# Optimization experiments

Hardware: AMD Instinct MI355X
Metric: run time of the kernel (lower is better)

Reference implementation:

```python
import jax, jax.numpy as jnp
import numpy as np

NS, NV = 48, 10                    # scalar / vector multiplicities (cfg.ns, cfg.nv)
WN = NS * NS + NS * NV             # per-edge TP weight numel: paths 0e*0e->0e and 0e*1o->1o
OUT = NS + 3 * NV                  # out irreps 48x0e + 10x1o -> 78 dims
INV = float(1.0 / np.sqrt(NS))     # e3nn-style path normalization (fan_in = mul_in)
N_LIG, N_REC, N_ATOM = 2000, 2000, 15000
E_LL, E_RR, E_AA = 15000, 10000, 15000
E_LR, E_LA, E_AR = 5000, 8000, 8000


def setup_inputs() -> dict:
    key = jax.random.key(0)
    ks = jax.random.split(key, 40)
    f = lambda i, shape, s=1.0: jax.random.normal(ks[i], shape, dtype=jnp.float32) * s
    ii = lambda i, n, e: jax.random.randint(ks[i], (e,), 0, n, dtype=jnp.int32)
    w_s = (1.0 / (3 * NS)) ** 0.5
    return {
        'lig_x': f(0, (N_LIG, NS)), 'rec_x': f(1, (N_REC, NS)), 'atom_x': f(2, (N_ATOM, NS)),
        'll_attr': f(3, (E_LL, NS)), 'rr_attr': f(4, (E_RR, NS)), 'aa_attr': f(5, (E_AA, NS)),
        'lr_attr': f(6, (E_LR, NS)), 'la_attr': f(7, (E_LA, NS)), 'ar_attr': f(8, (E_AR, NS)),
        'll_sh': f(9, (E_LL, 9)), 'rr_sh': f(10, (E_RR, 9)), 'aa_sh': f(11, (E_AA, 9)),
        'lr_sh': f(12, (E_LR, 9)), 'la_sh': f(13, (E_LA, 9)), 'ar_sh': f(14, (E_AR, 9)),
        'mlp_w1': f(15, (9, 3 * NS, 3 * NS), w_s), 'mlp_b1': jnp.zeros((9, 3 * NS), jnp.float32),
        'mlp_w2': f(16, (9, 3 * NS, 3 * NS), w_s), 'mlp_b2': jnp.zeros((9, 3 * NS), jnp.float32),
        'mlp_w3': f(17, (9, 3 * NS, WN), w_s), 'mlp_b3': jnp.zeros((9, WN), jnp.float32),
        'll_src': ii(18, N_LIG, E_LL), 'll_dst': ii(19, N_LIG, E_LL),
        'rr_src': ii(20, N_REC, E_RR), 'rr_dst': ii(21, N_REC, E_RR),
        'aa_src': ii(22, N_ATOM, E_AA), 'aa_dst': ii(23, N_ATOM, E_AA),
        'lr_lig': ii(24, N_LIG, E_LR), 'lr_rec': ii(25, N_REC, E_LR),
        'la_lig': ii(26, N_LIG, E_LA), 'la_atom': ii(27, N_ATOM, E_LA),
        'ar_atom': ii(28, N_ATOM, E_AR), 'ar_rec': ii(29, N_REC, E_AR),
    }


def _tp_conv(src_x, dst_x, e_attr, e_sh, src_idx, dst_idx, n_dst, w1, b1, w2, b2, w3, b3):
    """FullyConnectedTensorProductConv: per-edge MLP -> TP weights, CG tensor
    product of gathered source features with edge SH, mean scatter to dst."""
    fs = src_x[src_idx]                                          # (E, ns) gather
    z = jnp.concatenate([e_attr, fs, dst_x[dst_idx]], axis=-1)
    h = jax.nn.relu(z @ w1 + b1)
    h = jax.nn.relu(h @ w2 + b2)
    w = h @ w3 + b3                                              # (E, WN) edge-conditioned TP weights
    w0 = w[:, : NS * NS].reshape(-1, NS, NS)                     # 0e x 0e -> 0e path
    wv = w[:, NS * NS :].reshape(-1, NS, NV)                     # 0e x 1o -> 1o path
    out0 = jnp.einsum('ei,eio->eo', fs, w0) * e_sh[:, :1] * INV  # (E, ns)
    outv = jnp.einsum('ei,eiv,em->evm', fs, wv, e_sh[:, 1:4]) * INV  # (E, nv, 3)
    msg = jnp.concatenate([out0, outv.reshape(-1, NV * 3)], axis=-1)
    agg = jax.ops.segment_sum(msg, dst_idx, num_segments=n_dst)
    deg = jax.ops.segment_sum(jnp.ones((msg.shape[0], 1), msg.dtype), dst_idx, num_segments=n_dst)
    return agg / jnp.maximum(deg, 1.0)                           # mean reduction


def reference(lig_x, rec_x, atom_x, ll_attr, rr_attr, aa_attr, lr_attr, la_attr, ar_attr,
              ll_sh, rr_sh, aa_sh, lr_sh, la_sh, ar_sh,
              mlp_w1, mlp_b1, mlp_w2, mlp_b2, mlp_w3, mlp_b3,
              ll_src, ll_dst, rr_src, rr_dst, aa_src, aa_dst,
              lr_lig, lr_rec, la_lig, la_atom, ar_atom, ar_rec):
    P = lambda c: (mlp_w1[c], mlp_b1[c], mlp_w2[c], mlp_b2[c], mlp_w3[c], mlp_b3[c])
    # one interaction layer = 9 structurally distinct convs (lig/rec/atom intra + 6 cross dirs)
    lig_u = (_tp_conv(lig_x, lig_x, ll_attr, ll_sh, ll_src, ll_dst, N_LIG, *P(0))
           + _tp_conv(rec_x, lig_x, lr_attr, lr_sh, lr_rec, lr_lig, N_LIG, *P(1))
           + _tp_conv(atom_x, lig_x, la_attr, la_sh, la_atom, la_lig, N_LIG, *P(2)))
    rec_u = (_tp_conv(lig_x, rec_x, lr_attr, lr_sh, lr_lig, lr_rec, N_REC, *P(3))
           + _tp_conv(rec_x, rec_x, rr_attr, rr_sh, rr_src, rr_dst, N_REC, *P(4))
           + _tp_conv(atom_x, rec_x, ar_attr, ar_sh, ar_atom, ar_rec, N_REC, *P(5)))
    atom_u = (_tp_conv(lig_x, atom_x, la_attr, la_sh, la_lig, la_atom, N_ATOM, *P(6))
            + _tp_conv(rec_x, atom_x, ar_attr, ar_sh, ar_rec, ar_atom, N_ATOM, *P(7))
            + _tp_conv(atom_x, atom_x, aa_attr, aa_sh, aa_src, aa_dst, N_ATOM, *P(8)))
    pad = lambda x: jnp.pad(x, ((0, 0), (0, OUT - NS)))          # residual: pad scalars to out irreps
    return jnp.concatenate([pad(lig_x) + lig_u, pad(rec_x) + rec_u, pad(atom_x) + atom_u], axis=0)
```

## Files before the change

kernel.cpp:

```cpp
#include <hip/hip_runtime.h>


namespace {

constexpr int NCONV = 9;
constexpr int ETOT  = 82000;
constexpr float INV = 0.14433756729740643f;

constexpr int EC[NCONV]     = {15000,5000,8000,5000,10000,8000,8000,8000,15000};
constexpr int NBLKC[NCONV]  = {118,40,63,40,79,63,63,63,118};
constexpr int EOFF[NCONV]   = {0,15000,20000,28000,33000,43000,51000,59000,67000};
constexpr int DEGOFF[NCONV] = {0,2000,4000,6000,8000,10000,12000,27000,42000};
constexpr int NBLK_TOT = 647;

typedef _Float16 f16;
typedef __attribute__((ext_vector_type(8))) _Float16 f16x8;
typedef __attribute__((ext_vector_type(4))) float f32x4;

#define MFMA(a, b, c) __builtin_amdgcn_mfma_f32_16x16x32_f16((a), (b), (c), 0, 0, 0)

struct ConvPtrs {
  const float* src_x[NCONV];
  const float* dst_x[NCONV];
  const float* attr[NCONV];
  const float* sh[NCONV];
  const int*   sidx[NCONV];
  const int*   didx[NCONV];
};

}

__device__ __forceinline__ int conv_decode(int bid, int& rem) {
  int c = 0; rem = bid;
  while (c < NCONV - 1 && rem >= NBLKC[c]) { rem -= NBLKC[c]; ++c; }
  return c;
}

__global__ __launch_bounds__(64) void prep_w12(
    const float* __restrict__ w1, const float* __restrict__ b1,
    const float* __restrict__ w2, const float* __restrict__ b2,
    f16* __restrict__ w1f, f16* __restrict__ w2f) {
  const int b = blockIdx.x;
  const int sel = b >= 405, bb = sel ? b - 405 : b;
  const int c = bb / 45, r2 = bb % 45, cb = r2 / 5, s = r2 % 5;
  const float* w  = sel ? w2 : w1;
  const float* bi = sel ? b2 : b1;
  f16* dst = (sel ? w2f : w1f) + ((size_t)(c * 9 + cb) * 5 + s) * 512;
  const int l = threadIdx.x;
  const int n = cb * 16 + (l & 15);
  f16x8 pack;
#pragma unroll
  for (int j = 0; j < 8; ++j) {
    const int k = s * 32 + ((l >> 4) << 3) + j;
    float v = 0.f;
    if (k < 144)       v = w[((size_t)c * 144 + k) * 144 + n];
    else if (k == 144) v = bi[c * 144 + n];
    pack[j] = (f16)v;
  }
  ((f16x8*)dst)[l] = pack;
}

__global__ __launch_bounds__(256) void prep_w3k(
    const float* __restrict__ w3, const float* __restrict__ b3,
    f16* __restrict__ w3f) {
  const int b = blockIdx.x;
  const int c = b / 48, i = b % 48;
  const float* wc = w3 + (size_t)c * 144 * 2784;
  const float* bc = b3 + (size_t)c * 2784;
  f16* dst = w3f + (size_t)(c * 48 + i) * 20 * 512;
#pragma unroll 1
  for (int it = 0; it < 40; ++it) {
    const int f = it * 256 + threadIdx.x;
    const int s = f >> 11, g2 = f & 2047, cb = g2 >> 9, l = (g2 >> 3) & 63, j = f & 7;
    const int k = s * 32 + ((l >> 4) << 3) + j;
    const int col = cb * 16 + (l & 15);
    float v = 0.f;
    if (k <= 144) {
      const float* src = (k == 144) ? bc : (wc + (size_t)k * 2784);
      if (col < 48)      v = src[i * 48 + col];
      else if (col < 58) v = src[2304 + i * 10 + (col - 48)];
    }
    dst[f] = (f16)v;
  }
}

__global__ __launch_bounds__(256) void deg_kernel(ConvPtrs P, float* __restrict__ deg) {
  const int gid = blockIdx.x * 256 + threadIdx.x;
  if (gid >= ETOT) return;
  int c = 0;
  while (c < NCONV - 1 && gid >= EOFF[c + 1]) ++c;
  const int e = gid - EOFF[c];
  atomicAdd(&deg[DEGOFF[c] + P.didx[c][e]], 1.0f);
}

__global__ __launch_bounds__(256) void resid_kernel(
    const float* __restrict__ lig, const float* __restrict__ rec,
    const float* __restrict__ atom, float* __restrict__ out) {
  const int gid = blockIdx.x * 256 + threadIdx.x;
  if (gid >= 19000 * 78) return;
  const int row = gid / 78, j = gid - row * 78;
  const float* x; int node;
  if (row < 2000)      { x = lig;  node = row; }
  else if (row < 4000) { x = rec;  node = row - 2000; }
  else                 { x = atom; node = row - 4000; }
  out[gid] = (j < 48) ? x[(size_t)node * 48 + j] : 0.f;
}

template<int NCB, int CB0>
__device__ __forceinline__ void layer_mm(
    const f16x8* __restrict__ Av, const f16x8* __restrict__ wv,
    int c, int lane, int wr, f32x4 acc[4][5]) {
  f16x8 B[NCB][5];
#pragma unroll
  for (int cb = 0; cb < NCB; ++cb)
#pragma unroll
    for (int s = 0; s < 5; ++s)
      B[cb][s] = wv[((size_t)(c * 9 + CB0 + cb) * 5 + s) * 64 + lane];
#pragma unroll
  for (int rb = 0; rb < 4; ++rb)
#pragma unroll
    for (int cb = 0; cb < NCB; ++cb) acc[rb][cb] = (f32x4)0.0f;
#pragma unroll
  for (int s = 0; s < 5; ++s) {
    f16x8 A[4];
#pragma unroll
    for (int rb = 0; rb < 4; ++rb) A[rb] = Av[((wr * 4 + rb) * 5 + s) * 64 + lane];
#pragma unroll
    for (int rb = 0; rb < 4; ++rb)
#pragma unroll
      for (int cb = 0; cb < NCB; ++cb)
        acc[rb][cb] = MFMA(A[rb], B[cb][s], acc[rb][cb]);
  }
}

template<int NCB, int CB0>
__device__ __forceinline__ void layer_wb(const f32x4 acc[4][5], f16* __restrict__ At,
                                         int lane, int wr) {
#pragma unroll
  for (int cb = 0; cb < NCB; ++cb) {
    const int k = (CB0 + cb) * 16 + (lane & 15);
    const int s = k >> 5, g = (k >> 3) & 3, j = k & 7;
#pragma unroll
    for (int rb = 0; rb < 4; ++rb)
#pragma unroll
      for (int r = 0; r < 4; ++r) {
        const int row = ((lane >> 4) << 2) + r;
        At[((((wr * 4 + rb) * 5 + s) * 4 + g) * 16 + row) * 8 + j] =
            (f16)fmaxf(acc[rb][cb][r], 0.f);
      }
  }
}

#define BILIN_STEP(i, CUR, NXT)                                                   \
  {                                                                               \
    if ((i) + 1 < 48) {                                                           \
      const size_t fb = (size_t)(c * 48 + (i) + 1) * 20;                          \
      _Pragma("unroll") for (int s = 0; s < 5; ++s)                               \
        _Pragma("unroll") for (int cb = 0; cb < 2; ++cb)                          \
          Bb##NXT[cb][s] = w3v[(fb + s * 4 + (wc * 2 + cb)) * 64 + lane];         \
    }                                                                             \
    f32x4 T[4][2];                                                                \
    _Pragma("unroll") for (int rb = 0; rb < 4; ++rb)                              \
      _Pragma("unroll") for (int cb = 0; cb < 2; ++cb) T[rb][cb] = (f32x4)0.0f;   \
    _Pragma("unroll") for (int s = 0; s < 5; ++s)                                 \
      _Pragma("unroll") for (int rb = 0; rb < 4; ++rb)                            \
        _Pragma("unroll") for (int cb = 0; cb < 2; ++cb)                          \
          T[rb][cb] = MFMA(Af[rb][s], Bb##CUR[cb][s], T[rb][cb]);                 \
    _Pragma("unroll") for (int rb = 0; rb < 4; ++rb) {                            \
      const f32x4 fs4 =                                                           \
          *(const f32x4*)&fst[i][wr * 64 + rb * 16 + ((lane >> 4) << 2)];         \
      _Pragma("unroll") for (int cb = 0; cb < 2; ++cb)                            \
        msg[rb][cb] += fs4 * T[rb][cb];                                           \
    }                                                                             \
  }

__global__ __launch_bounds__(256, 2) void fused_conv(
    ConvPtrs P, const f16* __restrict__ w1f, const f16* __restrict__ w2f,
    const f16* __restrict__ w3f, const float* __restrict__ deg,
    float* __restrict__ out) {
  __shared__ f16   Atile[20480];
  __shared__ float fst[48][128];
  __shared__ float shb[128][4];
  __shared__ int   sidb[128], dstb[128];
  __shared__ float invdegb[128];

  int rem; const int c = conv_decode(blockIdx.x, rem);
  const int E = EC[c], e0 = rem * 128;
  const int tid = threadIdx.x, lane = tid & 63, w = tid >> 6;
  const int wr = w >> 1, wc = w & 1;

  if (tid < 128) {
    int ec = e0 + tid; if (ec >= E) ec = E - 1;
    sidb[tid] = P.sidx[c][ec];
    const int d = P.didx[c][ec]; dstb[tid] = d;
    const float* shp = P.sh[c] + (size_t)ec * 9;
    shb[tid][0] = shp[0]; shb[tid][1] = shp[1];
    shb[tid][2] = shp[2]; shb[tid][3] = shp[3];
    invdegb[tid] = 1.f / fmaxf(deg[DEGOFF[c] + d], 1.f);
  }
  __syncthreads();

  {
    const float* attr = P.attr[c];
    const float* sx = P.src_x[c];
    const float* dx = P.dst_x[c];
#pragma unroll 1
    for (int it = 0; it < 10; ++it) {
      const int u = it * 256 + tid, j8 = u >> 7, e = u & 127;
      int ec = e0 + e; if (ec >= E) ec = E - 1;
      float v[8];
      if (j8 < 6) {
        const float* p = attr + (size_t)ec * 48 + j8 * 8;
#pragma unroll
        for (int t = 0; t < 8; ++t) v[t] = p[t];
      } else if (j8 < 12) {
        const float* p = sx + (size_t)sidb[e] * 48 + (j8 - 6) * 8;
#pragma unroll
        for (int t = 0; t < 8; ++t) v[t] = p[t];
#pragma unroll
        for (int t = 0; t < 8; ++t) fst[(j8 - 6) * 8 + t][e] = v[t];
      } else if (j8 < 18) {
        const float* p = dx + (size_t)dstb[e] * 48 + (j8 - 12) * 8;
#pragma unroll
        for (int t = 0; t < 8; ++t) v[t] = p[t];
      } else if (j8 == 18) {
        v[0] = 1.f;
#pragma unroll
        for (int t = 1; t < 8; ++t) v[t] = 0.f;
      } else {
#pragma unroll
        for (int t = 0; t < 8; ++t) v[t] = 0.f;
      }
      f16x8 h;
#pragma unroll
      for (int t = 0; t < 8; ++t) h[t] = (f16)v[t];
      const int s = j8 >> 2, g = j8 & 3, rbg = e >> 4, row = e & 15;
      ((f16x8*)Atile)[((rbg * 5 + s) * 4 + g) * 16 + row] = h;
    }
  }
  __syncthreads();

  const f16x8* Av  = (const f16x8*)Atile;
  const f16x8* w1v = (const f16x8*)w1f;
  const f16x8* w2v = (const f16x8*)w2f;
  const f16x8* w3v = (const f16x8*)w3f;

  f32x4 acc[4][5];
  if (wc == 0) layer_mm<5, 0>(Av, w1v, c, lane, wr, acc);
  else         layer_mm<4, 5>(Av, w1v, c, lane, wr, acc);
  __syncthreads();
  if (wc == 0) layer_wb<5, 0>(acc, Atile, lane, wr);
  else         layer_wb<4, 5>(acc, Atile, lane, wr);
  __syncthreads();
  if (wc == 0) layer_mm<5, 0>(Av, w2v, c, lane, wr, acc);
  else         layer_mm<4, 5>(Av, w2v, c, lane, wr, acc);
  __syncthreads();
  if (wc == 0) layer_wb<5, 0>(acc, Atile, lane, wr);
  else         layer_wb<4, 5>(acc, Atile, lane, wr);
  __syncthreads();

  f16x8 Af[4][5];
#pragma unroll
  for (int rb = 0; rb < 4; ++rb)
#pragma unroll
    for (int s = 0; s < 5; ++s)
      Af[rb][s] = Av[((wr * 4 + rb) * 5 + s) * 64 + lane];

  f32x4 msg[4][2];
#pragma unroll
  for (int rb = 0; rb < 4; ++rb)
#pragma unroll
    for (int cb = 0; cb < 2; ++cb) msg[rb][cb] = (f32x4)0.0f;

  f16x8 Bb0[2][5], Bb1[2][5];
  {
    const size_t fb = (size_t)(c * 48) * 20;
#pragma unroll
    for (int s = 0; s < 5; ++s)
#pragma unroll
      for (int cb = 0; cb < 2; ++cb)
        Bb0[cb][s] = w3v[(fb + s * 4 + (wc * 2 + cb)) * 64 + lane];
  }
#pragma unroll 1
  for (int ii = 0; ii < 48; ii += 2) {
    BILIN_STEP(ii, 0, 1);
    BILIN_STEP(ii + 1, 1, 0);
  }

  const int outbase = (c < 3) ? 0 : (c < 6 ? 2000 : 4000);
#pragma unroll
  for (int rb = 0; rb < 4; ++rb)
#pragma unroll
    for (int r = 0; r < 4; ++r) {
      const int el = wr * 64 + rb * 16 + ((lane >> 4) << 2) + r;
      if (e0 + el >= E) continue;
      const float sc = invdegb[el] * INV;
      float* op = out + ((size_t)outbase + dstb[el]) * 78;
      const float s0 = shb[el][0], s1 = shb[el][1], s2 = shb[el][2], s3 = shb[el][3];
#pragma unroll
      for (int cb = 0; cb < 2; ++cb) {
        const int col = (wc * 2 + cb) * 16 + (lane & 15);
        const float v = msg[rb][cb][r] * sc;
        if (col < 48) {
          atomicAdd(op + col, v * s0);
        } else if (col < 58) {
          const int vv = col - 48;
          atomicAdd(op + 48 + vv * 3 + 0, v * s1);
          atomicAdd(op + 48 + vv * 3 + 1, v * s2);
          atomicAdd(op + 48 + vv * 3 + 2, v * s3);
        }
      }
    }
}

extern "C" void kernel_launch(void* const* d_in, const int* in_sizes, int n_in,
                              void* d_out, int out_size, void* d_ws, size_t ws_size,
                              hipStream_t stream) {
  (void)in_sizes; (void)n_in; (void)out_size; (void)ws_size;
  const float* lig_x  = (const float*)d_in[0];
  const float* rec_x  = (const float*)d_in[1];
  const float* atom_x = (const float*)d_in[2];
  const float* attr_ll = (const float*)d_in[3];
  const float* attr_rr = (const float*)d_in[4];
  const float* attr_aa = (const float*)d_in[5];
  const float* attr_lr = (const float*)d_in[6];
  const float* attr_la = (const float*)d_in[7];
  const float* attr_ar = (const float*)d_in[8];
  const float* sh_ll = (const float*)d_in[9];
  const float* sh_rr = (const float*)d_in[10];
  const float* sh_aa = (const float*)d_in[11];
  const float* sh_lr = (const float*)d_in[12];
  const float* sh_la = (const float*)d_in[13];
  const float* sh_ar = (const float*)d_in[14];
  const float* w1 = (const float*)d_in[15];
  const float* b1 = (const float*)d_in[16];
  const float* w2 = (const float*)d_in[17];
  const float* b2 = (const float*)d_in[18];
  const float* w3 = (const float*)d_in[19];
  const float* b3 = (const float*)d_in[20];
  const int* ll_src = (const int*)d_in[21];
  const int* ll_dst = (const int*)d_in[22];
  const int* rr_src = (const int*)d_in[23];
  const int* rr_dst = (const int*)d_in[24];
  const int* aa_src = (const int*)d_in[25];
  const int* aa_dst = (const int*)d_in[26];
  const int* lr_lig = (const int*)d_in[27];
  const int* lr_rec = (const int*)d_in[28];
  const int* la_lig = (const int*)d_in[29];
  const int* la_atom = (const int*)d_in[30];
  const int* ar_atom = (const int*)d_in[31];
  const int* ar_rec  = (const int*)d_in[32];

  f16* w1f = (f16*)d_ws;
  f16* w2f = w1f + 207360;
  f16* w3f = w2f + 207360;
  float* deg = (float*)(w3f + 4423680);

  ConvPtrs P;
  const float* SX[NCONV] = {lig_x, rec_x, atom_x, lig_x, rec_x, atom_x, lig_x, rec_x, atom_x};
  const float* DX[NCONV] = {lig_x, lig_x, lig_x, rec_x, rec_x, rec_x, atom_x, atom_x, atom_x};
  const float* AT[NCONV] = {attr_ll, attr_lr, attr_la, attr_lr, attr_rr, attr_ar, attr_la, attr_ar, attr_aa};
  const float* SH[NCONV] = {sh_ll, sh_lr, sh_la, sh_lr, sh_rr, sh_ar, sh_la, sh_ar, sh_aa};
  const int*   SI[NCONV] = {ll_src, lr_rec, la_atom, lr_lig, rr_src, ar_atom, la_lig, ar_rec, aa_src};
  const int*   DI[NCONV] = {ll_dst, lr_lig, la_lig, lr_rec, rr_dst, ar_rec, la_atom, ar_atom, aa_dst};
  for (int cc = 0; cc < NCONV; ++cc) {
    P.src_x[cc] = SX[cc]; P.dst_x[cc] = DX[cc]; P.attr[cc] = AT[cc];
    P.sh[cc] = SH[cc]; P.sidx[cc] = SI[cc]; P.didx[cc] = DI[cc];
  }

  prep_w12<<<810, 64, 0, stream>>>(w1, b1, w2, b2, w1f, w2f);
  prep_w3k<<<432, 256, 0, stream>>>(w3, b3, w3f);
  hipMemsetAsync(deg, 0, 57000 * sizeof(float), stream);
  deg_kernel<<<(ETOT + 255) / 256, 256, 0, stream>>>(P, deg);
  resid_kernel<<<(19000 * 78 + 255) / 256, 256, 0, stream>>>(lig_x, rec_x, atom_x, (float*)d_out);
  fused_conv<<<NBLK_TOT, 256, 0, stream>>>(P, w1f, w2f, w3f, deg, (float*)d_out);
}
```

Before: 212.2 us.

## Stream W3 tiles through LDS with async loads and raise occupancy to three blocks

```diff
diff --git a/kernel.cpp b/kernel.cpp
--- a/kernel.cpp
+++ b/kernel.cpp
@@ -15,6 +15,7 @@
 
 typedef _Float16 f16;
 typedef __attribute__((ext_vector_type(8))) _Float16 f16x8;
+typedef __attribute__((ext_vector_type(4))) _Float16 f16x4;
 typedef __attribute__((ext_vector_type(4))) float f32x4;
 
 #define MFMA(a, b, c) __builtin_amdgcn_mfma_f32_16x16x32_f16((a), (b), (c), 0, 0, 0)
@@ -34,6 +35,16 @@
   int c = 0; rem = bid;
   while (c < NCONV - 1 && rem >= NBLKC[c]) { rem -= NBLKC[c]; ++c; }
   return c;
+}
+
+__device__ __forceinline__ void gld_lds16(const void* g, void* l) {
+  __builtin_amdgcn_global_load_lds(
+      (const __attribute__((address_space(1))) void*)g,
+      (__attribute__((address_space(3))) void*)l, 16, 0, 0);
+}
+
+__device__ __forceinline__ f32x4 cvt4(f16x4 h) {
+  return (f32x4){(float)h[0], (float)h[1], (float)h[2], (float)h[3]};
 }
 
 __global__ __launch_bounds__(64) void prep_w12(
@@ -110,18 +121,16 @@
 __device__ __forceinline__ void layer_mm(
     const f16x8* __restrict__ Av, const f16x8* __restrict__ wv,
     int c, int lane, int wr, f32x4 acc[4][5]) {
-  f16x8 B[NCB][5];
-#pragma unroll
-  for (int cb = 0; cb < NCB; ++cb)
-#pragma unroll
-    for (int s = 0; s < 5; ++s)
-      B[cb][s] = wv[((size_t)(c * 9 + CB0 + cb) * 5 + s) * 64 + lane];
 #pragma unroll
   for (int rb = 0; rb < 4; ++rb)
 #pragma unroll
     for (int cb = 0; cb < NCB; ++cb) acc[rb][cb] = (f32x4)0.0f;
 #pragma unroll
   for (int s = 0; s < 5; ++s) {
+    f16x8 B[NCB];
+#pragma unroll
+    for (int cb = 0; cb < NCB; ++cb)
+      B[cb] = wv[((size_t)(c * 9 + CB0 + cb) * 5 + s) * 64 + lane];
     f16x8 A[4];
 #pragma unroll
     for (int rb = 0; rb < 4; ++rb) A[rb] = Av[((wr * 4 + rb) * 5 + s) * 64 + lane];
@@ -129,7 +138,7 @@
     for (int rb = 0; rb < 4; ++rb)
 #pragma unroll
       for (int cb = 0; cb < NCB; ++cb)
-        acc[rb][cb] = MFMA(A[rb], B[cb][s], acc[rb][cb]);
+        acc[rb][cb] = MFMA(A[rb], B[cb], acc[rb][cb]);
   }
 }
 
@@ -151,38 +160,15 @@
   }
 }
 
-#define BILIN_STEP(i, CUR, NXT)                                                   \
-  {                                                                               \
-    if ((i) + 1 < 48) {                                                           \
-      const size_t fb = (size_t)(c * 48 + (i) + 1) * 20;                          \
-      _Pragma("unroll") for (int s = 0; s < 5; ++s)                               \
-        _Pragma("unroll") for (int cb = 0; cb < 2; ++cb)                          \
-          Bb##NXT[cb][s] = w3v[(fb + s * 4 + (wc * 2 + cb)) * 64 + lane];         \
-    }                                                                             \
-    f32x4 T[4][2];                                                                \
-    _Pragma("unroll") for (int rb = 0; rb < 4; ++rb)                              \
-      _Pragma("unroll") for (int cb = 0; cb < 2; ++cb) T[rb][cb] = (f32x4)0.0f;   \
-    _Pragma("unroll") for (int s = 0; s < 5; ++s)                                 \
-      _Pragma("unroll") for (int rb = 0; rb < 4; ++rb)                            \
-        _Pragma("unroll") for (int cb = 0; cb < 2; ++cb)                          \
-          T[rb][cb] = MFMA(Af[rb][s], Bb##CUR[cb][s], T[rb][cb]);                 \
-    _Pragma("unroll") for (int rb = 0; rb < 4; ++rb) {                            \
-      const f32x4 fs4 =                                                           \
-          *(const f32x4*)&fst[i][wr * 64 + rb * 16 + ((lane >> 4) << 2)];         \
-      _Pragma("unroll") for (int cb = 0; cb < 2; ++cb)                            \
-        msg[rb][cb] += fs4 * T[rb][cb];                                           \
-    }                                                                             \
-  }
-
-__global__ __launch_bounds__(256, 2) void fused_conv(
+__global__ __launch_bounds__(256, 3) void fused_conv(
     ConvPtrs P, const f16* __restrict__ w1f, const f16* __restrict__ w2f,
     const f16* __restrict__ w3f, const float* __restrict__ deg,
     float* __restrict__ out) {
-  __shared__ f16   Atile[20480];
-  __shared__ float fst[48][128];
-  __shared__ float shb[128][4];
-  __shared__ int   sidb[128], dstb[128];
-  __shared__ float invdegb[128];
+  __shared__ __align__(16) char smem[54272];
+  f16* Atile = (f16*)smem;
+  f16 (*fst)[128] = (f16 (*)[128])(smem + 40960);
+  int* sidb = (int*)(smem + 53248);
+  int* dstb = (int*)(smem + 53760);
 
   int rem; const int c = conv_decode(blockIdx.x, rem);
   const int E = EC[c], e0 = rem * 128;
@@ -192,11 +178,7 @@
   if (tid < 128) {
     int ec = e0 + tid; if (ec >= E) ec = E - 1;
     sidb[tid] = P.sidx[c][ec];
-    const int d = P.didx[c][ec]; dstb[tid] = d;
-    const float* shp = P.sh[c] + (size_t)ec * 9;
-    shb[tid][0] = shp[0]; shb[tid][1] = shp[1];
-    shb[tid][2] = shp[2]; shb[tid][3] = shp[3];
-    invdegb[tid] = 1.f / fmaxf(deg[DEGOFF[c] + d], 1.f);
+    dstb[tid] = P.didx[c][ec];
   }
   __syncthreads();
 
@@ -218,7 +200,7 @@
 #pragma unroll
         for (int t = 0; t < 8; ++t) v[t] = p[t];
 #pragma unroll
-        for (int t = 0; t < 8; ++t) fst[(j8 - 6) * 8 + t][e] = v[t];
+        for (int t = 0; t < 8; ++t) fst[(j8 - 6) * 8 + t][e] = (f16)v[t];
       } else if (j8 < 18) {
         const float* p = dx + (size_t)dstb[e] * 48 + (j8 - 12) * 8;
 #pragma unroll
@@ -240,20 +222,17 @@
   }
   __syncthreads();
 
-  const f16x8* Av  = (const f16x8*)Atile;
-  const f16x8* w1v = (const f16x8*)w1f;
-  const f16x8* w2v = (const f16x8*)w2f;
-  const f16x8* w3v = (const f16x8*)w3f;
+  const f16x8* Av = (const f16x8*)Atile;
 
   f32x4 acc[4][5];
-  if (wc == 0) layer_mm<5, 0>(Av, w1v, c, lane, wr, acc);
-  else         layer_mm<4, 5>(Av, w1v, c, lane, wr, acc);
+  if (wc == 0) layer_mm<5, 0>(Av, (const f16x8*)w1f, c, lane, wr, acc);
+  else         layer_mm<4, 5>(Av, (const f16x8*)w1f, c, lane, wr, acc);
   __syncthreads();
   if (wc == 0) layer_wb<5, 0>(acc, Atile, lane, wr);
   else         layer_wb<4, 5>(acc, Atile, lane, wr);
   __syncthreads();
-  if (wc == 0) layer_mm<5, 0>(Av, w2v, c, lane, wr, acc);
-  else         layer_mm<4, 5>(Av, w2v, c, lane, wr, acc);
+  if (wc == 0) layer_mm<5, 0>(Av, (const f16x8*)w2f, c, lane, wr, acc);
+  else         layer_mm<4, 5>(Av, (const f16x8*)w2f, c, lane, wr, acc);
   __syncthreads();
   if (wc == 0) layer_wb<5, 0>(acc, Atile, lane, wr);
   else         layer_wb<4, 5>(acc, Atile, lane, wr);
@@ -265,6 +244,11 @@
 #pragma unroll
     for (int s = 0; s < 5; ++s)
       Af[rb][s] = Av[((wr * 4 + rb) * 5 + s) * 64 + lane];
+  __syncthreads();
+
+  const f16* __restrict__ w3c = w3f + (size_t)(c * 48) * 10240;
+  f16* buf0 = Atile;
+  f16* buf1 = Atile + 10240;
 
   f32x4 msg[4][2];
 #pragma unroll
@@ -272,31 +256,64 @@
 #pragma unroll
     for (int cb = 0; cb < 2; ++cb) msg[rb][cb] = (f32x4)0.0f;
 
-  f16x8 Bb0[2][5], Bb1[2][5];
-  {
-    const size_t fb = (size_t)(c * 48) * 20;
-#pragma unroll
-    for (int s = 0; s < 5; ++s)
-#pragma unroll
-      for (int cb = 0; cb < 2; ++cb)
-        Bb0[cb][s] = w3v[(fb + s * 4 + (wc * 2 + cb)) * 64 + lane];
-  }
+#pragma unroll
+  for (int q = 0; q < 5; ++q) {
+    const int chunk = q * 4 + w;
+    gld_lds16(w3c + chunk * 512 + lane * 8, buf0 + chunk * 512);
+  }
+  __syncthreads();
+
 #pragma unroll 1
-  for (int ii = 0; ii < 48; ii += 2) {
-    BILIN_STEP(ii, 0, 1);
-    BILIN_STEP(ii + 1, 1, 0);
+  for (int i = 0; i < 48; ++i) {
+    f16* bcur = (i & 1) ? buf1 : buf0;
+    f16* bnxt = (i & 1) ? buf0 : buf1;
+    if (i + 1 < 48) {
+      const f16* gsrc = w3c + (size_t)(i + 1) * 10240;
+#pragma unroll
+      for (int q = 0; q < 5; ++q) {
+        const int chunk = q * 4 + w;
+        gld_lds16(gsrc + chunk * 512 + lane * 8, bnxt + chunk * 512);
+      }
+    }
+    f16x4 fsh[4];
+#pragma unroll
+    for (int rb = 0; rb < 4; ++rb)
+      fsh[rb] = *(const f16x4*)&fst[i][wr * 64 + rb * 16 + ((lane >> 4) << 2)];
+
+    const f16x8* bv = (const f16x8*)bcur;
+#pragma unroll
+    for (int cb = 0; cb < 2; ++cb) {
+      f16x8 Bf[5];
+#pragma unroll
+      for (int s = 0; s < 5; ++s) Bf[s] = bv[(s * 4 + wc * 2 + cb) * 64 + lane];
+      f32x4 T[4];
+#pragma unroll
+      for (int rb = 0; rb < 4; ++rb) T[rb] = (f32x4)0.0f;
+#pragma unroll
+      for (int s = 0; s < 5; ++s)
+#pragma unroll
+        for (int rb = 0; rb < 4; ++rb) T[rb] = MFMA(Af[rb][s], Bf[s], T[rb]);
+#pragma unroll
+      for (int rb = 0; rb < 4; ++rb) msg[rb][cb] += cvt4(fsh[rb]) * T[rb];
+    }
+    __syncthreads();
   }
 
   const int outbase = (c < 3) ? 0 : (c < 6 ? 2000 : 4000);
+  const float* __restrict__ shp = P.sh[c];
+  const float* __restrict__ degc = deg + DEGOFF[c];
 #pragma unroll
   for (int rb = 0; rb < 4; ++rb)
 #pragma unroll
     for (int r = 0; r < 4; ++r) {
       const int el = wr * 64 + rb * 16 + ((lane >> 4) << 2) + r;
-      if (e0 + el >= E) continue;
-      const float sc = invdegb[el] * INV;
-      float* op = out + ((size_t)outbase + dstb[el]) * 78;
-      const float s0 = shb[el][0], s1 = shb[el][1], s2 = shb[el][2], s3 = shb[el][3];
+      const int ec = e0 + el;
+      if (ec >= E) continue;
+      const int dst = dstb[el];
+      const float sc = INV / fmaxf(degc[dst], 1.f);
+      const float* shq = shp + (size_t)ec * 9;
+      const float s0 = shq[0], s1 = shq[1], s2 = shq[2], s3 = shq[3];
+      float* op = out + ((size_t)outbase + dst) * 78;
 #pragma unroll
       for (int cb = 0; cb < 2; ++cb) {
         const int col = (wc * 2 + cb) * 16 + (lane & 15);
```

New measurement: 202.9 us. 1.05x faster.
